# Kernel optimization log

Measured on AMD Instinct MI355X. Metric: run time of the kernel, lower is better.

The kernel has to match this reference:

```python
import jax, jax.numpy as jnp
import numpy as np

MODES = 2
LC = 4
N = 6000
KNN = 10
NODES = 64
CH = MODES ** 2
M = N * 2 * (KNN + 1)  # total candidate couplings


def setup_inputs() -> dict:
    key = jax.random.key(0)
    ks = jax.random.split(key, 6)
    return {
        "CK_inputs": jax.random.normal(ks[0], (N, 2 * (KNN + 1), 3), dtype=jnp.float32),
        "W_in": jax.random.normal(ks[1], (3, NODES), dtype=jnp.float32) * 0.1,
        "b_in": jnp.zeros((NODES,), dtype=jnp.float32),
        "W_hid": jax.random.normal(ks[2], (LC - 1, NODES, NODES), dtype=jnp.float32) * 0.1,
        "b_hid": jnp.zeros((LC - 1, NODES), dtype=jnp.float32),
        "W_out": jax.random.normal(ks[3], (NODES, CH), dtype=jnp.float32) * 0.1,
        "b_out": jnp.zeros((CH,), dtype=jnp.float32),
        "coo": jax.random.randint(ks[4], (2, M), 0, N, dtype=jnp.int32),
    }


def _mlp(x, W_in, b_in, W_hid, b_hid, W_out, b_out):
    # MLP: 3 -> 64, (LC-1) hidden 64->64 layers, 64 -> CH; ReLU activations.
    h = jax.nn.relu(x @ W_in + b_in)
    for i in range(W_hid.shape[0]):  # small fixed layer count
        h = jax.nn.relu(h @ W_hid[i] + b_hid[i])
    return h @ W_out + b_out  # [M, CH]


def reference(CK_inputs, W_in, b_in, W_hid, b_hid, W_out, b_out, coo):
    C_stripped = _mlp(CK_inputs.reshape(-1, 3), W_in, b_in, W_hid, b_hid, W_out, b_out)  # [M, CH]
    D = MODES * N
    # Original: for channel ch = mi*MODES+mj, scatter C_stripped[:, ch] at indices coo*MODES+mj
    # (mj added to BOTH row and col, replicating the source exactly). Indices are
    # independent of mi, so sum over mi first, then one scatter-add per mj.
    vals = C_stripped.reshape(-1, MODES, MODES).sum(axis=1)  # [M, MODES]; axis1=mi, axis2=mj
    dense = jnp.zeros((D, D), dtype=CK_inputs.dtype)
    for mj in range(MODES):
        idx = coo * MODES + mj  # [2, M]
        dense = dense.at[idx[0], idx[1]].add(vals[:, mj])
    return dense
```

## Files before the change

### kernel.cpp

```cpp
#include <hip/hip_runtime.h>
#include <stdint.h>

#define NN    6000
#define KNNC  10
#define MM    (NN * 2 * (KNNC + 1))
#define DD    (2 * NN)
#define BLK   256

#define NV          ((long long)DD * DD / 4)
#define FILL_BLOCKS 4096
#define MLP_BLOCKS  512
#define NWAVES      (MLP_BLOCKS * 4)
#define NGRP        ((MM + 3) / 4)

__global__ __launch_bounds__(BLK) void fill_out(float* __restrict__ out) {
    float4 z = make_float4(0.f, 0.f, 0.f, 0.f);
    float4* outv = (float4*)out;
    long long i = (long long)blockIdx.x * BLK + threadIdx.x;
    const long long stride = (long long)FILL_BLOCKS * BLK;
    for (; i < NV; i += stride) outv[i] = z;
}

__device__ __forceinline__ float rlane(float v, int l) {
    return __builtin_bit_cast(float,
        __builtin_amdgcn_readlane(__builtin_bit_cast(int, v), l));
}

__global__ __launch_bounds__(BLK, 2) void mlp_scatter(
    const float* __restrict__ CK,
    const float* __restrict__ Win,
    const float* __restrict__ bin,
    const float* __restrict__ Whid,
    const float* __restrict__ bhid,
    const float* __restrict__ Wout,
    const float* __restrict__ bout,
    const int*   __restrict__ coo,
    float* __restrict__ out)
{
    const int tid  = threadIdx.x;
    const int lane = tid & 63;
    const int gwid = blockIdx.x * 4 + (tid >> 6);

    float W0[64], W1[64], W2[64];
#pragma unroll
    for (int k = 0; k < 64; k++) W0[k] = Whid[k * 64 + lane];
#pragma unroll
    for (int k = 0; k < 64; k++) W1[k] = Whid[4096 + k * 64 + lane];
#pragma unroll
    for (int k = 0; k < 64; k++) W2[k] = Whid[8192 + k * 64 + lane];

    const float wi0 = Win[lane], wi1 = Win[64 + lane], wi2 = Win[128 + lane];
    const float b0  = bin[lane];
    const float bh0 = bhid[lane], bh1 = bhid[64 + lane], bh2 = bhid[128 + lane];
    const float4 wo = ((const float4*)Wout)[lane];
    const float wc0 = wo.x + wo.z;
    const float wc1 = wo.y + wo.w;
    const float bo0 = bout[0] + bout[2];
    const float bo1 = bout[1] + bout[3];

#define HIDDEN(W, BH)                                                   \
    {                                                                   \
        float g0 = (BH), g1 = (BH), g2 = (BH), g3 = (BH);               \
        _Pragma("unroll")                                               \
        for (int k = 0; k < 64; k++) {                                  \
            g0 = fmaf(W[k], rlane(h0, k), g0);                          \
            g1 = fmaf(W[k], rlane(h1, k), g1);                          \
            g2 = fmaf(W[k], rlane(h2, k), g2);                          \
            g3 = fmaf(W[k], rlane(h3, k), g3);                          \
        }                                                               \
        h0 = fmaxf(g0, 0.f); h1 = fmaxf(g1, 0.f);                       \
        h2 = fmaxf(g2, 0.f); h3 = fmaxf(g3, 0.f);                       \
    }

    for (int grp = gwid; grp < NGRP; grp += NWAVES) {
        const int rowbase = grp * 4;

        float vck = 0.f;
        const int cidx = rowbase * 3 + lane;
        if (lane < 12 && cidx < MM * 3) vck = CK[cidx];

        float h0 = fmaxf(fmaf(rlane(vck, 2), wi2,
                         fmaf(rlane(vck, 1), wi1,
                         fmaf(rlane(vck, 0), wi0, b0))), 0.f);
        float h1 = fmaxf(fmaf(rlane(vck, 5), wi2,
                         fmaf(rlane(vck, 4), wi1,
                         fmaf(rlane(vck, 3), wi0, b0))), 0.f);
        float h2 = fmaxf(fmaf(rlane(vck, 8), wi2,
                         fmaf(rlane(vck, 7), wi1,
                         fmaf(rlane(vck, 6), wi0, b0))), 0.f);
        float h3 = fmaxf(fmaf(rlane(vck, 11), wi2,
                         fmaf(rlane(vck, 10), wi1,
                         fmaf(rlane(vck, 9), wi0, b0))), 0.f);

        HIDDEN(W0, bh0)
        HIDDEN(W1, bh1)
        HIDDEN(W2, bh2)

        float p00 = h0 * wc0, p01 = h0 * wc1;
        float p10 = h1 * wc0, p11 = h1 * wc1;
        float p20 = h2 * wc0, p21 = h2 * wc1;
        float p30 = h3 * wc0, p31 = h3 * wc1;
#pragma unroll
        for (int m = 32; m; m >>= 1) {
            p00 += __shfl_xor(p00, m, 64);  p01 += __shfl_xor(p01, m, 64);
            p10 += __shfl_xor(p10, m, 64);  p11 += __shfl_xor(p11, m, 64);
            p20 += __shfl_xor(p20, m, 64);  p21 += __shfl_xor(p21, m, 64);
            p30 += __shfl_xor(p30, m, 64);  p31 += __shfl_xor(p31, m, 64);
        }

        float a0 = lane == 0 ? p00 : lane == 1 ? p10 : lane == 2 ? p20 : p30;
        float a1 = lane == 0 ? p01 : lane == 1 ? p11 : lane == 2 ? p21 : p31;
        a0 += bo0;
        a1 += bo1;
        const int myrow = rowbase + lane;
        if (lane < 4 && myrow < MM) {
            const int r2 = coo[myrow] * 2;
            const int c2 = coo[MM + myrow] * 2;
            const long long f0 = (long long)r2 * DD + c2;
            atomicAdd(out + f0, a0);
            atomicAdd(out + f0 + DD + 1, a1);
        }
    }
#undef HIDDEN
}

extern "C" void kernel_launch(void* const* d_in, const int* in_sizes, int n_in,
                              void* d_out, int out_size, void* d_ws, size_t ws_size,
                              hipStream_t stream) {
    const float* CK   = (const float*)d_in[0];
    const float* Win  = (const float*)d_in[1];
    const float* bin  = (const float*)d_in[2];
    const float* Whid = (const float*)d_in[3];
    const float* bhid = (const float*)d_in[4];
    const float* Wout = (const float*)d_in[5];
    const float* bout = (const float*)d_in[6];
    const int* coo    = (const int*)d_in[7];
    float* out        = (float*)d_out;

    fill_out<<<FILL_BLOCKS, BLK, 0, stream>>>(out);
    mlp_scatter<<<MLP_BLOCKS, BLK, 0, stream>>>(
        CK, Win, bin, Whid, bhid, Wout, bout, coo, out);
}
```

Measured before the change: 736.8 us.

## Bucket MLP outputs by row and fuse dense zero-fill with scatter

The MLP kernel no longer scatters atomics into the full 576 MB dense output. It appends (col, value) entries to per-row buckets in workspace, with an overflow list for rows past capacity. A new per-row kernel zeroes each pair of output rows and applies that row's bucketed entries with atomics. A final kernel applies the overflow entries. The aim is to replace scattered global atomics into a cold 144M-element matrix with local, cache-resident updates right after the row is written. The cost is extra workspace traffic, and entries beyond the fixed overflow cap are silently dropped.

New measurement: 735.9 us. About the same (-0.1%).

```diff
diff --git a/kernel.cpp b/kernel.cpp
--- a/kernel.cpp
+++ b/kernel.cpp
@@ -7,26 +7,22 @@
 #define DD    (2 * NN)
 #define BLK   256
 
-#define NV          ((long long)DD * DD / 4)
-#define FILL_BLOCKS 4096
-#define MLP_BLOCKS  512
-#define NWAVES      (MLP_BLOCKS * 4)
-#define NGRP        ((MM + 3) / 4)
+#define MLP_BLOCKS 512
+#define NWAVES     (MLP_BLOCKS * 4)
+#define NGRP       (MM / 4)
 
-__global__ __launch_bounds__(BLK) void fill_out(float* __restrict__ out) {
-    float4 z = make_float4(0.f, 0.f, 0.f, 0.f);
-    float4* outv = (float4*)out;
-    long long i = (long long)blockIdx.x * BLK + threadIdx.x;
-    const long long stride = (long long)FILL_BLOCKS * BLK;
-    for (; i < NV; i += stride) outv[i] = z;
-}
+#define CAP     96
+#define OVF_IDX 8064
+#define MAX_OVF 4096
+#define BUCKET_OFF  32768
+#define OVF_OFF     (BUCKET_OFF + 6000 * CAP * 16)
 
 __device__ __forceinline__ float rlane(float v, int l) {
     return __builtin_bit_cast(float,
         __builtin_amdgcn_readlane(__builtin_bit_cast(int, v), l));
 }
 
-__global__ __launch_bounds__(BLK, 2) void mlp_scatter(
+__global__ __launch_bounds__(BLK, 1) void mlp_bucket(
     const float* __restrict__ CK,
     const float* __restrict__ Win,
     const float* __restrict__ bin,
@@ -35,7 +31,9 @@
     const float* __restrict__ Wout,
     const float* __restrict__ bout,
     const int*   __restrict__ coo,
-    float* __restrict__ out)
+    int*    __restrict__ cnt,
+    float4* __restrict__ bucket,
+    int4*   __restrict__ ovf)
 {
     const int tid  = threadIdx.x;
     const int lane = tid & 63;
@@ -76,8 +74,7 @@
         const int rowbase = grp * 4;
 
         float vck = 0.f;
-        const int cidx = rowbase * 3 + lane;
-        if (lane < 12 && cidx < MM * 3) vck = CK[cidx];
+        if (lane < 12) vck = CK[rowbase * 3 + lane];
 
         float h0 = fmaxf(fmaf(rlane(vck, 2), wi2,
                          fmaf(rlane(vck, 1), wi1,
@@ -108,20 +105,58 @@
             p30 += __shfl_xor(p30, m, 64);  p31 += __shfl_xor(p31, m, 64);
         }
 
-        float a0 = lane == 0 ? p00 : lane == 1 ? p10 : lane == 2 ? p20 : p30;
-        float a1 = lane == 0 ? p01 : lane == 1 ? p11 : lane == 2 ? p21 : p31;
-        a0 += bo0;
-        a1 += bo1;
-        const int myrow = rowbase + lane;
-        if (lane < 4 && myrow < MM) {
-            const int r2 = coo[myrow] * 2;
+        if (lane < 4) {
+            const float a0 = (lane == 0 ? p00 : lane == 1 ? p10 : lane == 2 ? p20 : p30) + bo0;
+            const float a1 = (lane == 0 ? p01 : lane == 1 ? p11 : lane == 2 ? p21 : p31) + bo1;
+            const int myrow = rowbase + lane;
+            const int r  = coo[myrow];
             const int c2 = coo[MM + myrow] * 2;
-            const long long f0 = (long long)r2 * DD + c2;
-            atomicAdd(out + f0, a0);
-            atomicAdd(out + f0 + DD + 1, a1);
+            const int slot = atomicAdd(&cnt[r], 1);
+            if (slot < CAP) {
+                bucket[r * CAP + slot] = make_float4(__int_as_float(c2), a0, a1, 0.f);
+            } else {
+                const int o = atomicAdd(&cnt[OVF_IDX], 1);
+                if (o < MAX_OVF)
+                    ovf[o] = make_int4(r, c2, __float_as_int(a0), __float_as_int(a1));
+            }
         }
     }
 #undef HIDDEN
+}
+
+__global__ __launch_bounds__(BLK) void fill_patch(
+    const int*    __restrict__ cnt,
+    const float4* __restrict__ bucket,
+    float*        __restrict__ out)
+{
+    const int b = blockIdx.x;
+    float* rowbase = out + (long long)b * 2 * DD;
+    float4* dst = (float4*)rowbase;
+    const float4 z = make_float4(0.f, 0.f, 0.f, 0.f);
+    for (int i = threadIdx.x; i < 6000; i += BLK) dst[i] = z;
+    __syncthreads();
+
+    const int n = min(cnt[b], CAP);
+    for (int t = threadIdx.x; t < n; t += BLK) {
+        float4 e = bucket[b * CAP + t];
+        const int c2 = __float_as_int(e.x);
+        atomicAdd(rowbase + c2, e.y);
+        atomicAdd(rowbase + DD + c2 + 1, e.z);
+    }
+}
+
+__global__ __launch_bounds__(BLK) void ovf_apply(
+    const int*  __restrict__ cnt,
+    const int4* __restrict__ ovf,
+    float*      __restrict__ out)
+{
+    const int n = min(cnt[OVF_IDX], MAX_OVF);
+    const int t = blockIdx.x * BLK + threadIdx.x;
+    if (t >= n) return;
+    int4 e = ovf[t];
+    float* rowbase = out + (long long)e.x * 2 * DD;
+    atomicAdd(rowbase + e.y, __int_as_float(e.z));
+    atomicAdd(rowbase + DD + e.y + 1, __int_as_float(e.w));
 }
 
 extern "C" void kernel_launch(void* const* d_in, const int* in_sizes, int n_in,
@@ -137,7 +172,13 @@
     const int* coo    = (const int*)d_in[7];
     float* out        = (float*)d_out;
 
-    fill_out<<<FILL_BLOCKS, BLK, 0, stream>>>(out);
-    mlp_scatter<<<MLP_BLOCKS, BLK, 0, stream>>>(
-        CK, Win, bin, Whid, bhid, Wout, bout, coo, out);
+    int*    cnt    = (int*)d_ws;
+    float4* bucket = (float4*)((char*)d_ws + BUCKET_OFF);
+    int4*   ovf    = (int4*)((char*)d_ws + OVF_OFF);
+
+    hipMemsetAsync(cnt, 0, 32768, stream);
+    mlp_bucket<<<MLP_BLOCKS, BLK, 0, stream>>>(
+        CK, Win, bin, Whid, bhid, Wout, bout, coo, cnt, bucket, ovf);
+    fill_patch<<<NN, BLK, 0, stream>>>(cnt, bucket, out);
+    ovf_apply<<<(MAX_OVF + BLK - 1) / BLK, BLK, 0, stream>>>(cnt, ovf, out);
 }
```
